# Performance work log

Measured on AMD Instinct MI355X. Metric: run time of the kernel, lower is better.

The kernel has to match this reference:

```python
import jax, jax.numpy as jnp
import numpy as np

B, N, D, H = 4, 16384, 64, 8
MIN_FREQ = 1.0 / 64.0
SCALE = 1.0
EPS = 1e-5


def layernorm(x):
    # LayerNorm over last (head-feature) dim, no affine, biased variance (torch default)
    m = jnp.mean(x, axis=-1, keepdims=True)
    v = jnp.mean(jnp.square(x - m), axis=-1, keepdims=True)
    return (x - m) * jax.lax.rsqrt(v + EPS)


def rope_freqs(pos):
    # pos: [b, n, 1] 1-D coordinates -> freqs [b, n, D]
    inv_freq = 1.0 / (10000.0 ** (jnp.arange(0, D, 2, dtype=jnp.float32) / D))  # [D/2]
    t = pos[..., 0] * (SCALE / MIN_FREQ)                                         # [b, n]
    f = t[..., None] * inv_freq                                                  # [b, n, D/2]
    return jnp.concatenate([f, f], axis=-1)                                      # [b, n, D]


def rotate_half(x):
    x1, x2 = jnp.split(x, 2, axis=-1)
    return jnp.concatenate([-x2, x1], axis=-1)


def apply_rope(x, freqs):
    # x: [b, h, n, d], freqs: [b, n, d]
    c = jnp.cos(freqs)[:, None]
    s = jnp.sin(freqs)[:, None]
    return x * c + rotate_half(x) * s


def setup_inputs() -> dict:
    key = jax.random.key(0)
    ks = jax.random.split(key, 6)
    gain = 1.0 / D
    return {
        "x": jax.random.normal(ks[0], (B, N, D), dtype=jnp.float32),
        "pos": jax.random.uniform(ks[1], (B, N, 1), dtype=jnp.float32),
        "Wq": jax.random.normal(ks[2], (D, D * H), dtype=jnp.float32) * gain,
        "Wk": jax.random.normal(ks[3], (D, D * H), dtype=jnp.float32) * gain,
        "Wv": jax.random.normal(ks[4], (D, D * H), dtype=jnp.float32) * gain,
        "Wo": jax.random.normal(ks[5], (D * H, D), dtype=jnp.float32) * gain,
    }


def reference(x, pos, Wq, Wk, Wv, Wo):
    b, n, _ = x.shape

    def proj(W):
        # [b, n, d] @ [d, h*d] -> [b, h, n, d]
        y = jnp.einsum("bnd,de->bne", x, W)
        return y.reshape(b, n, H, D).transpose(0, 2, 1, 3)

    q, k, v = proj(Wq), proj(Wk), proj(Wv)

    # galerkin: layernorm k and v (no mask path)
    k = layernorm(k)
    v = layernorm(v)

    # RoPE on q, k
    freqs = rope_freqs(pos)
    q = apply_rope(q, freqs)
    k = apply_rope(k, freqs)

    # linear attention: z = q @ (k^T v) / n
    kv = jnp.einsum("bhnd,bhne->bhde", k, v)          # [b, h, d, d]
    z = jnp.einsum("bhnd,bhde->bhne", q, kv) / n      # [b, h, n, d]
    z = z.transpose(0, 2, 1, 3).reshape(b, n, H * D)  # [b, n, h*d]

    return jnp.einsum("bne,ed->bnd", z, Wo)           # out_proj (dropout=0)
```

## Files before the change

### kernel.cpp

```cpp
#include <hip/hip_runtime.h>

#define B_ 4
#define N_ 16384
#define D_ 64
#define H_ 8
#define E_ 512
#define NCHUNK 32
#define NTILES (N_ / 64)

typedef __attribute__((ext_vector_type(8))) short short8;
typedef __attribute__((ext_vector_type(4))) float f32x4;
typedef __attribute__((ext_vector_type(2))) unsigned int uint32x2;

__device__ __forceinline__ unsigned short f2b(float f) {
    unsigned u = __float_as_uint(f);
    return (unsigned short)((u + 0x7fffu + ((u >> 16) & 1u)) >> 16);
}

__device__ __forceinline__ unsigned cvtpk(float a, float b) {
    unsigned r;
    asm("v_cvt_pk_bf16_f32 %0, %1, %2" : "=v"(r) : "v"(a), "v"(b));
    return r;
}

template<int CTRL>
__device__ __forceinline__ float dppadd(float x) {
    int y = __builtin_amdgcn_update_dpp(0, __float_as_int(x), CTRL, 0xF, 0xF, true);
    return x + __int_as_float(y);
}
__device__ __forceinline__ float rowsum16(float x) {
    x = dppadd<0xB1>(x);
    x = dppadd<0x4E>(x);
    x = dppadd<0x141>(x);
    x = dppadd<0x140>(x);
    return x;
}

__global__ __launch_bounds__(256) void k_prep(
    const float* __restrict__ x,
    const float* __restrict__ Wq, const float* __restrict__ Wk,
    const float* __restrict__ Wv,
    unsigned short* __restrict__ WqB, unsigned short* __restrict__ WkB,
    unsigned short* __restrict__ WvB,
    unsigned short* __restrict__ xblob)
{
    const int bid = blockIdx.x, tid = threadIdx.x;
    if (bid < 384) {
        int mat = bid >> 7, sub = bid & 127;
        const float* src = (mat == 0) ? Wq : (mat == 1) ? Wk : Wv;
        unsigned short* dst = (mat == 0) ? WqB : (mat == 1) ? WkB : WvB;
        int id = sub * 256 + tid;
        int kin = id >> 9, f = id & 511;
        int h = f >> 6, feat = f & 63;
        int nt = feat >> 4, cc = feat & 15;
        int half = kin >> 5, qd = (kin >> 3) & 3, e = kin & 7;
        dst[(size_t)h * 4096 + (((nt * 2 + half) * 64 + qd * 16 + cc) * 8) + e]
            = f2b(src[id]);
        return;
    }
    int idx = (bid - 384) * 256 + tid;
    int lane = idx & 63, fr = (idx >> 6) & 1, tb = (idx >> 7) & 1023, b = idx >> 17;
    int cc = lane & 15, qd = lane >> 4;
    const float* src = &x[((size_t)b * N_ + tb * 16 + cc) * 64 + fr * 32 + qd * 8];
    float4 v0 = *(const float4*)src;
    float4 v1 = *(const float4*)(src + 4);
    ushort4 u0, u1;
    u0.x = f2b(v0.x); u0.y = f2b(v0.y); u0.z = f2b(v0.z); u0.w = f2b(v0.w);
    u1.x = f2b(v1.x); u1.y = f2b(v1.y); u1.z = f2b(v1.z); u1.w = f2b(v1.w);
    *(ushort4*)&xblob[(size_t)idx * 8]     = u0;
    *(ushort4*)&xblob[(size_t)idx * 8 + 4] = u1;
}

__global__ __launch_bounds__(256, 4) void k_kv(
    const unsigned short* __restrict__ xblob,
    const float* __restrict__ pos,
    const unsigned short* __restrict__ WkB,
    const unsigned short* __restrict__ WvB,
    float* __restrict__ kv_part)
{
    const int b = blockIdx.z, h = blockIdx.y, chunk = blockIdx.x;
    const int tid  = threadIdx.x;
    const int lane = tid & 63;
    const int w    = tid >> 6;
    const int c    = lane & 15;
    const int quad = lane >> 4;
    const int m0   = w * 16;

    __shared__ unsigned short kbuf[64 * 72];
    __shared__ unsigned short vbuf[64 * 72];
    __shared__ unsigned short wkl[4096];
    __shared__ unsigned short wvl[4096];

    {
        const float4* srcK = (const float4*)(WkB + (size_t)h * 4096);
        const float4* srcV = (const float4*)(WvB + (size_t)h * 4096);
        float4* dstK = (float4*)wkl;
        float4* dstV = (float4*)wvl;
        #pragma unroll
        for (int i = 0; i < 2; ++i) {
            dstK[tid + i * 256] = srcK[tid + i * 256];
            dstV[tid + i * 256] = srcV[tid + i * 256];
        }
    }

    const float invf_lo = exp2f(-0.4152410118609203f * (float)c);
    const float invf_hi = invf_lo * 0.01f;

    f32x4 akv[4];
    #pragma unroll
    for (int nt = 0; nt < 4; ++nt) akv[nt] = (f32x4){0.f, 0.f, 0.f, 0.f};

    short8 a0, a1;
    float tp[4];
    {
        int tb = chunk * 4 + w;
        const unsigned short* xb = xblob + (size_t)((b * 1024 + tb) * 2) * 512 + lane * 8;
        a0 = *(const short8*)&xb[0];
        a1 = *(const short8*)&xb[512];
        #pragma unroll
        for (int r = 0; r < 4; ++r)
            tp[r] = pos[(size_t)b * N_ + chunk * 64 + m0 + quad * 4 + r] * 64.0f;
    }
    __syncthreads();

    for (int tile = chunk; tile < NTILES; tile += NCHUNK) {
        f32x4 ak[4], av[4];
        #pragma unroll
        for (int nt = 0; nt < 4; ++nt) {
            short8 bk0 = *(const short8*)&wkl[(nt * 2 + 0) * 512 + lane * 8];
            short8 bk1 = *(const short8*)&wkl[(nt * 2 + 1) * 512 + lane * 8];
            f32x4 z = {0.f, 0.f, 0.f, 0.f};
            z = __builtin_amdgcn_mfma_f32_16x16x32_bf16(a0, bk0, z, 0, 0, 0);
            ak[nt] = __builtin_amdgcn_mfma_f32_16x16x32_bf16(a1, bk1, z, 0, 0, 0);
            short8 bv0 = *(const short8*)&wvl[(nt * 2 + 0) * 512 + lane * 8];
            short8 bv1 = *(const short8*)&wvl[(nt * 2 + 1) * 512 + lane * 8];
            f32x4 y = {0.f, 0.f, 0.f, 0.f};
            y = __builtin_amdgcn_mfma_f32_16x16x32_bf16(a0, bv0, y, 0, 0, 0);
            av[nt] = __builtin_amdgcn_mfma_f32_16x16x32_bf16(a1, bv1, y, 0, 0, 0);
        }

        float cl[4], sl[4], ch[4], sh[4];
        #pragma unroll
        for (int r = 0; r < 4; ++r) {
            float al = tp[r] * invf_lo, ah = tp[r] * invf_hi;
            cl[r] = __cosf(al); sl[r] = __sinf(al);
            ch[r] = __cosf(ah); sh[r] = __sinf(ah);
        }

        const int tn = tile + NCHUNK;
        if (tn < NTILES) {
            int tb = tn * 4 + w;
            const unsigned short* xb = xblob + (size_t)((b * 1024 + tb) * 2) * 512 + lane * 8;
            a0 = *(const short8*)&xb[0];
            a1 = *(const short8*)&xb[512];
            #pragma unroll
            for (int r = 0; r < 4; ++r)
                tp[r] = pos[(size_t)b * N_ + tn * 64 + m0 + quad * 4 + r] * 64.0f;
        }
        __builtin_amdgcn_sched_barrier(0);

        #pragma unroll
        for (int r = 0; r < 4; ++r) {
            float sk  = ak[0][r] + ak[1][r] + ak[2][r] + ak[3][r];
            float sk2 = ak[0][r]*ak[0][r] + ak[1][r]*ak[1][r] + ak[2][r]*ak[2][r] + ak[3][r]*ak[3][r];
            float sv  = av[0][r] + av[1][r] + av[2][r] + av[3][r];
            float sv2 = av[0][r]*av[0][r] + av[1][r]*av[1][r] + av[2][r]*av[2][r] + av[3][r]*av[3][r];
            sk = rowsum16(sk); sk2 = rowsum16(sk2);
            sv = rowsum16(sv); sv2 = rowsum16(sv2);
            float mk = sk * (1.0f / 64.0f);
            float rk = rsqrtf(sk2 * (1.0f / 64.0f) - mk * mk + 1e-5f);
            float mv = sv * (1.0f / 64.0f);
            float rv = rsqrtf(sv2 * (1.0f / 64.0f) - mv * mv + 1e-5f);
            #pragma unroll
            for (int nt = 0; nt < 4; ++nt) {
                ak[nt][r] = (ak[nt][r] - mk) * rk;
                av[nt][r] = (av[nt][r] - mv) * rv;
            }
        }

        #pragma unroll
        for (int r = 0; r < 4; ++r) {
            float lo0 = ak[0][r], hi0 = ak[2][r];
            ak[0][r] = lo0 * cl[r] - hi0 * sl[r];
            ak[2][r] = hi0 * cl[r] + lo0 * sl[r];
            float lo1 = ak[1][r], hi1 = ak[3][r];
            ak[1][r] = lo1 * ch[r] - hi1 * sh[r];
            ak[3][r] = hi1 * ch[r] + lo1 * sh[r];
        }

        __syncthreads();

        #pragma unroll
        for (int nt = 0; nt < 4; ++nt) {
            uint32x2 kk, vv;
            kk[0] = cvtpk(ak[nt][0], ak[nt][1]);
            kk[1] = cvtpk(ak[nt][2], ak[nt][3]);
            vv[0] = cvtpk(av[nt][0], av[nt][1]);
            vv[1] = cvtpk(av[nt][2], av[nt][3]);
            *(uint32x2*)&kbuf[(nt * 16 + c) * 72 + m0 + quad * 4] = kk;
            *(uint32x2*)&vbuf[(nt * 16 + c) * 72 + m0 + quad * 4] = vv;
        }
        __syncthreads();

        short8 ka0 = *(const short8*)&kbuf[(m0 + c) * 72 + quad * 8];
        short8 ka1 = *(const short8*)&kbuf[(m0 + c) * 72 + 32 + quad * 8];
        #pragma unroll
        for (int nt = 0; nt < 4; ++nt) {
            short8 vb0 = *(const short8*)&vbuf[(nt * 16 + c) * 72 + quad * 8];
            short8 vb1 = *(const short8*)&vbuf[(nt * 16 + c) * 72 + 32 + quad * 8];
            akv[nt] = __builtin_amdgcn_mfma_f32_16x16x32_bf16(ka0, vb0, akv[nt], 0, 0, 0);
            akv[nt] = __builtin_amdgcn_mfma_f32_16x16x32_bf16(ka1, vb1, akv[nt], 0, 0, 0);
        }
    }

    float* dst = kv_part + ((size_t)(b * H_ + h) * NCHUNK + chunk) * 4096;
    #pragma unroll
    for (int nt = 0; nt < 4; ++nt)
        #pragma unroll
        for (int r = 0; r < 4; ++r)
            dst[(size_t)(16 * w + quad * 4 + r) * 64 + nt * 16 + c] = akv[nt][r];
}

__global__ __launch_bounds__(256) void k_m(
    const float* __restrict__ kv_part,
    const float* __restrict__ Wo,
    unsigned short* __restrict__ MTB)
{
    const int h = blockIdx.x, b = blockIdx.y, s = blockIdx.z;
    const int tid = threadIdx.x;
    __shared__ float kvs[8 * 65];
    __shared__ float wos[64 * 68];

    const float* src = kv_part + (size_t)(b * H_ + h) * NCHUNK * 4096 + s * 512;
    #pragma unroll
    for (int k = 0; k < 2; ++k) {
        int idx = tid + k * 256;
        float ssum = 0.f;
        #pragma unroll 8
        for (int ch = 0; ch < NCHUNK; ++ch) ssum += src[(size_t)ch * 4096 + idx];
        kvs[(idx >> 6) * 65 + (idx & 63)] = ssum;
    }
    for (int i = tid; i < 1024; i += 256) {
        int dp = i >> 4, j4 = (i & 15) * 4;
        *(float4*)&wos[dp * 68 + j4] = *(const float4*)&Wo[(size_t)(h * 64 + dp) * 64 + j4];
    }
    __syncthreads();

    const float inv_n = 1.0f / (float)N_;
    unsigned short* dst = MTB + (size_t)(b * H_ + h) * 4096;
    const int half = s >> 2, qd = s & 3;
    #pragma unroll
    for (int k = 0; k < 2; ++k) {
        int idx = tid + k * 256;
        int dl = idx >> 6, j = idx & 63;
        float acc = 0.f;
        #pragma unroll 8
        for (int e = 0; e < 64; ++e)
            acc += kvs[dl * 65 + e] * wos[e * 68 + j];
        int nt = j >> 4, cc = j & 15;
        dst[(((nt * 2 + half) * 64 + qd * 16 + cc) * 8) + dl] = f2b(acc * inv_n);
    }
}

__global__ __launch_bounds__(256, 3) void k_out(
    const unsigned short* __restrict__ xblob,
    const float* __restrict__ pos,
    const unsigned short* __restrict__ WqB,
    const unsigned short* __restrict__ MTB,
    float* __restrict__ out)
{
    const int b = blockIdx.y;
    const int n0 = blockIdx.x * 64;
    const int tid  = threadIdx.x;
    const int lane = tid & 63;
    const int w    = tid >> 6;
    const int c    = lane & 15;
    const int quad = lane >> 4;
    const int m0   = w * 16;

    __shared__ unsigned short qbuf[64 * 72];

    const int tb = blockIdx.x * 4 + w;
    const unsigned short* xb = xblob + (size_t)((b * 1024 + tb) * 2) * 512 + lane * 8;
    short8 a0 = *(const short8*)&xb[0];
    short8 a1 = *(const short8*)&xb[512];

    const unsigned short* wq0 = WqB + (size_t)lane * 8;
    const unsigned short* mt0 = MTB + (size_t)(b * H_) * 4096 + (size_t)lane * 8;
    short8 W[8], Mt[8];
    #pragma unroll
    for (int fr = 0; fr < 8; ++fr) W[fr]  = *(const short8*)&wq0[fr * 512];
    #pragma unroll
    for (int fr = 0; fr < 8; ++fr) Mt[fr] = *(const short8*)&mt0[fr * 512];
    __builtin_amdgcn_sched_barrier(0);

    const float invf_lo = exp2f(-0.4152410118609203f * (float)c);
    const float invf_hi = invf_lo * 0.01f;
    float csl[4], snl[4], csh[4], snh[4];
    #pragma unroll
    for (int r = 0; r < 4; ++r) {
        float tpv = pos[(size_t)b * N_ + n0 + m0 + quad * 4 + r] * 64.0f;
        float al = tpv * invf_lo, ah = tpv * invf_hi;
        csl[r] = __cosf(al); snl[r] = __sinf(al);
        csh[r] = __cosf(ah); snh[r] = __sinf(ah);
    }

    f32x4 oacc[4];
    #pragma unroll
    for (int nt = 0; nt < 4; ++nt) oacc[nt] = (f32x4){0.f, 0.f, 0.f, 0.f};

    #pragma unroll
    for (int h = 0; h < H_; ++h) {
        f32x4 aq[4];
        #pragma unroll
        for (int nt = 0; nt < 4; ++nt) {
            f32x4 z = {0.f, 0.f, 0.f, 0.f};
            z = __builtin_amdgcn_mfma_f32_16x16x32_bf16(a0, W[nt * 2 + 0], z, 0, 0, 0);
            aq[nt] = __builtin_amdgcn_mfma_f32_16x16x32_bf16(a1, W[nt * 2 + 1], z, 0, 0, 0);
        }

        if (h < H_ - 1) {
            #pragma unroll
            for (int fr = 0; fr < 8; ++fr)
                W[fr] = *(const short8*)&wq0[(size_t)(h + 1) * 4096 + fr * 512];
        }
        __builtin_amdgcn_sched_barrier(0);

        #pragma unroll
        for (int r = 0; r < 4; ++r) {
            float lo0 = aq[0][r], hi0 = aq[2][r];
            aq[0][r] = lo0 * csl[r] - hi0 * snl[r];
            aq[2][r] = hi0 * csl[r] + lo0 * snl[r];
            float lo1 = aq[1][r], hi1 = aq[3][r];
            aq[1][r] = lo1 * csh[r] - hi1 * snh[r];
            aq[3][r] = hi1 * csh[r] + lo1 * snh[r];
        }

        #pragma unroll
        for (int nt = 0; nt < 4; ++nt) {
            unsigned q01 = cvtpk(aq[nt][0], aq[nt][1]);
            unsigned q23 = cvtpk(aq[nt][2], aq[nt][3]);
            int base = (m0 + quad * 4) * 72 + nt * 16 + c;
            qbuf[base]       = (unsigned short)q01;
            qbuf[base + 72]  = (unsigned short)(q01 >> 16);
            qbuf[base + 144] = (unsigned short)q23;
            qbuf[base + 216] = (unsigned short)(q23 >> 16);
        }

        short8 qa0 = *(const short8*)&qbuf[(m0 + c) * 72 + quad * 8];
        short8 qa1 = *(const short8*)&qbuf[(m0 + c) * 72 + 32 + quad * 8];
        #pragma unroll
        for (int nt = 0; nt < 4; ++nt) {
            oacc[nt] = __builtin_amdgcn_mfma_f32_16x16x32_bf16(qa0, Mt[nt * 2 + 0], oacc[nt], 0, 0, 0);
            oacc[nt] = __builtin_amdgcn_mfma_f32_16x16x32_bf16(qa1, Mt[nt * 2 + 1], oacc[nt], 0, 0, 0);
        }

        if (h < H_ - 1) {
            #pragma unroll
            for (int fr = 0; fr < 8; ++fr)
                Mt[fr] = *(const short8*)&mt0[(size_t)(h + 1) * 4096 + fr * 512];
        }
        __builtin_amdgcn_sched_barrier(0);
    }

    #pragma unroll
    for (int nt = 0; nt < 4; ++nt)
        #pragma unroll
        for (int r = 0; r < 4; ++r)
            out[(size_t)(b * N_ + n0 + m0 + quad * 4 + r) * 64 + nt * 16 + c] = oacc[nt][r];
}

extern "C" void kernel_launch(void* const* d_in, const int* in_sizes, int n_in,
                              void* d_out, int out_size, void* d_ws, size_t ws_size,
                              hipStream_t stream)
{
    const float* x   = (const float*)d_in[0];
    const float* pos = (const float*)d_in[1];
    const float* Wq  = (const float*)d_in[2];
    const float* Wk  = (const float*)d_in[3];
    const float* Wv  = (const float*)d_in[4];
    const float* Wo  = (const float*)d_in[5];
    float* out = (float*)d_out;

    char* ws = (char*)d_ws;
    float* kv_part        = (float*)ws;
    unsigned short* MTB   = (unsigned short*)(ws + 16777216);
    unsigned short* WqB   = (unsigned short*)(ws + 17039360);
    unsigned short* WkB   = (unsigned short*)(ws + 17104896);
    unsigned short* WvB   = (unsigned short*)(ws + 17170432);
    unsigned short* xblob = (unsigned short*)(ws + 17235968);

    k_prep<<<dim3(2432), 256, 0, stream>>>(x, Wq, Wk, Wv,
                                           WqB, WkB, WvB, xblob);
    k_kv  <<<dim3(NCHUNK, H_, B_), 256, 0, stream>>>(xblob, pos, WkB, WvB, kv_part);
    k_m   <<<dim3(H_, B_, 8), 256, 0, stream>>>(kv_part, Wo, MTB);
    k_out <<<dim3(NTILES, B_), 256, 0, stream>>>(xblob, pos, WqB, MTB, out);
}
```

Measured before the change: 142.0 us.

## Run two tile streams per 512-thread kv block and reduce partials in LDS

The k_kv kernel now launches 512-thread blocks holding two independent groups of four waves. Each group processes its own strided tile stream with separate LDS k/v buffers, which raises the number of tile streams from 32 to 48 per (b,h). The two groups' kv accumulators are summed through LDS before writing, so there are only 24 partials per head, which shrinks the k_m reduction and the workspace. The grid gets fewer, larger blocks, and the two groups share __syncthreads barriers, which may couple their progress.

After: 190.0 us. +33.8%, slower.

```diff
diff --git a/kernel.cpp b/kernel.cpp
--- a/kernel.cpp
+++ b/kernel.cpp
@@ -5,7 +5,8 @@
 #define D_ 64
 #define H_ 8
 #define E_ 512
-#define NCHUNK 32
+#define NPART 24
+#define TSTREAMS 48
 #define NTILES (N_ / 64)
 
 typedef __attribute__((ext_vector_type(8))) short short8;
@@ -71,37 +72,30 @@
     *(ushort4*)&xblob[(size_t)idx * 8 + 4] = u1;
 }
 
-__global__ __launch_bounds__(256, 4) void k_kv(
+__global__ __launch_bounds__(512, 6) void k_kv(
     const unsigned short* __restrict__ xblob,
     const float* __restrict__ pos,
     const unsigned short* __restrict__ WkB,
     const unsigned short* __restrict__ WvB,
     float* __restrict__ kv_part)
 {
-    const int b = blockIdx.z, h = blockIdx.y, chunk = blockIdx.x;
+    const int b = blockIdx.z, h = blockIdx.y, bx = blockIdx.x;
     const int tid  = threadIdx.x;
     const int lane = tid & 63;
     const int w    = tid >> 6;
+    const int g    = w >> 2;
+    const int wl   = w & 3;
     const int c    = lane & 15;
     const int quad = lane >> 4;
-    const int m0   = w * 16;
-
-    __shared__ unsigned short kbuf[64 * 72];
-    __shared__ unsigned short vbuf[64 * 72];
+    const int m0   = wl * 16;
+
+    __shared__ unsigned short kbuf[2][64 * 72];
+    __shared__ unsigned short vbuf[2][64 * 72];
     __shared__ unsigned short wkl[4096];
     __shared__ unsigned short wvl[4096];
 
-    {
-        const float4* srcK = (const float4*)(WkB + (size_t)h * 4096);
-        const float4* srcV = (const float4*)(WvB + (size_t)h * 4096);
-        float4* dstK = (float4*)wkl;
-        float4* dstV = (float4*)wvl;
-        #pragma unroll
-        for (int i = 0; i < 2; ++i) {
-            dstK[tid + i * 256] = srcK[tid + i * 256];
-            dstV[tid + i * 256] = srcV[tid + i * 256];
-        }
-    }
+    ((float4*)wkl)[tid] = ((const float4*)(WkB + (size_t)h * 4096))[tid];
+    ((float4*)wvl)[tid] = ((const float4*)(WvB + (size_t)h * 4096))[tid];
 
     const float invf_lo = exp2f(-0.4152410118609203f * (float)c);
     const float invf_hi = invf_lo * 0.01f;
@@ -110,20 +104,21 @@
     #pragma unroll
     for (int nt = 0; nt < 4; ++nt) akv[nt] = (f32x4){0.f, 0.f, 0.f, 0.f};
 
+    const int tile0 = bx * 2 + g;
     short8 a0, a1;
     float tp[4];
     {
-        int tb = chunk * 4 + w;
+        int tb = tile0 * 4 + wl;
         const unsigned short* xb = xblob + (size_t)((b * 1024 + tb) * 2) * 512 + lane * 8;
         a0 = *(const short8*)&xb[0];
         a1 = *(const short8*)&xb[512];
         #pragma unroll
         for (int r = 0; r < 4; ++r)
-            tp[r] = pos[(size_t)b * N_ + chunk * 64 + m0 + quad * 4 + r] * 64.0f;
+            tp[r] = pos[(size_t)b * N_ + tile0 * 64 + m0 + quad * 4 + r] * 64.0f;
     }
     __syncthreads();
 
-    for (int tile = chunk; tile < NTILES; tile += NCHUNK) {
+    for (int tile = tile0; tile < NTILES; tile += TSTREAMS) {
         f32x4 ak[4], av[4];
         #pragma unroll
         for (int nt = 0; nt < 4; ++nt) {
@@ -147,9 +142,9 @@
             ch[r] = __cosf(ah); sh[r] = __sinf(ah);
         }
 
-        const int tn = tile + NCHUNK;
+        const int tn = tile + TSTREAMS;
         if (tn < NTILES) {
-            int tb = tn * 4 + w;
+            int tb = tn * 4 + wl;
             const unsigned short* xb = xblob + (size_t)((b * 1024 + tb) * 2) * 512 + lane * 8;
             a0 = *(const short8*)&xb[0];
             a1 = *(const short8*)&xb[512];
@@ -197,28 +192,42 @@
             kk[1] = cvtpk(ak[nt][2], ak[nt][3]);
             vv[0] = cvtpk(av[nt][0], av[nt][1]);
             vv[1] = cvtpk(av[nt][2], av[nt][3]);
-            *(uint32x2*)&kbuf[(nt * 16 + c) * 72 + m0 + quad * 4] = kk;
-            *(uint32x2*)&vbuf[(nt * 16 + c) * 72 + m0 + quad * 4] = vv;
+            *(uint32x2*)&kbuf[g][(nt * 16 + c) * 72 + m0 + quad * 4] = kk;
+            *(uint32x2*)&vbuf[g][(nt * 16 + c) * 72 + m0 + quad * 4] = vv;
         }
         __syncthreads();
 
-        short8 ka0 = *(const short8*)&kbuf[(m0 + c) * 72 + quad * 8];
-        short8 ka1 = *(const short8*)&kbuf[(m0 + c) * 72 + 32 + quad * 8];
-        #pragma unroll
-        for (int nt = 0; nt < 4; ++nt) {
-            short8 vb0 = *(const short8*)&vbuf[(nt * 16 + c) * 72 + quad * 8];
-            short8 vb1 = *(const short8*)&vbuf[(nt * 16 + c) * 72 + 32 + quad * 8];
+        short8 ka0 = *(const short8*)&kbuf[g][(m0 + c) * 72 + quad * 8];
+        short8 ka1 = *(const short8*)&kbuf[g][(m0 + c) * 72 + 32 + quad * 8];
+        #pragma unroll
+        for (int nt = 0; nt < 4; ++nt) {
+            short8 vb0 = *(const short8*)&vbuf[g][(nt * 16 + c) * 72 + quad * 8];
+            short8 vb1 = *(const short8*)&vbuf[g][(nt * 16 + c) * 72 + 32 + quad * 8];
             akv[nt] = __builtin_amdgcn_mfma_f32_16x16x32_bf16(ka0, vb0, akv[nt], 0, 0, 0);
             akv[nt] = __builtin_amdgcn_mfma_f32_16x16x32_bf16(ka1, vb1, akv[nt], 0, 0, 0);
         }
     }
 
-    float* dst = kv_part + ((size_t)(b * H_ + h) * NCHUNK + chunk) * 4096;
-    #pragma unroll
-    for (int nt = 0; nt < 4; ++nt)
-        #pragma unroll
-        for (int r = 0; r < 4; ++r)
-            dst[(size_t)(16 * w + quad * 4 + r) * 64 + nt * 16 + c] = akv[nt][r];
+    __syncthreads();
+    float* fbuf = (float*)kbuf;
+    if (g == 1) {
+        #pragma unroll
+        for (int nt = 0; nt < 4; ++nt)
+            #pragma unroll
+            for (int r = 0; r < 4; ++r)
+                fbuf[(size_t)(16 * wl + quad * 4 + r) * 64 + nt * 16 + c] = akv[nt][r];
+    }
+    __syncthreads();
+    if (g == 0) {
+        float* dst = kv_part + ((size_t)(b * H_ + h) * NPART + bx) * 4096;
+        #pragma unroll
+        for (int nt = 0; nt < 4; ++nt)
+            #pragma unroll
+            for (int r = 0; r < 4; ++r) {
+                int idx = (16 * wl + quad * 4 + r) * 64 + nt * 16 + c;
+                dst[idx] = akv[nt][r] + fbuf[idx];
+            }
+    }
 }
 
 __global__ __launch_bounds__(256) void k_m(
@@ -231,13 +240,13 @@
     __shared__ float kvs[8 * 65];
     __shared__ float wos[64 * 68];
 
-    const float* src = kv_part + (size_t)(b * H_ + h) * NCHUNK * 4096 + s * 512;
+    const float* src = kv_part + (size_t)(b * H_ + h) * NPART * 4096 + s * 512;
     #pragma unroll
     for (int k = 0; k < 2; ++k) {
         int idx = tid + k * 256;
         float ssum = 0.f;
-        #pragma unroll 8
-        for (int ch = 0; ch < NCHUNK; ++ch) ssum += src[(size_t)ch * 4096 + idx];
+        #pragma unroll 6
+        for (int ch = 0; ch < NPART; ++ch) ssum += src[(size_t)ch * 4096 + idx];
         kvs[(idx >> 6) * 65 + (idx & 63)] = ssum;
     }
     for (int i = tid; i < 1024; i += 256) {
@@ -384,15 +393,15 @@
 
     char* ws = (char*)d_ws;
     float* kv_part        = (float*)ws;
-    unsigned short* MTB   = (unsigned short*)(ws + 16777216);
-    unsigned short* WqB   = (unsigned short*)(ws + 17039360);
-    unsigned short* WkB   = (unsigned short*)(ws + 17104896);
-    unsigned short* WvB   = (unsigned short*)(ws + 17170432);
-    unsigned short* xblob = (unsigned short*)(ws + 17235968);
+    unsigned short* MTB   = (unsigned short*)(ws + 12582912);
+    unsigned short* WqB   = (unsigned short*)(ws + 12845056);
+    unsigned short* WkB   = (unsigned short*)(ws + 12910592);
+    unsigned short* WvB   = (unsigned short*)(ws + 12976128);
+    unsigned short* xblob = (unsigned short*)(ws + 13041664);
 
     k_prep<<<dim3(2432), 256, 0, stream>>>(x, Wq, Wk, Wv,
                                            WqB, WkB, WvB, xblob);
-    k_kv  <<<dim3(NCHUNK, H_, B_), 256, 0, stream>>>(xblob, pos, WkB, WvB, kv_part);
+    k_kv  <<<dim3(NPART, H_, B_), 512, 0, stream>>>(xblob, pos, WkB, WvB, kv_part);
     k_m   <<<dim3(H_, B_, 8), 256, 0, stream>>>(kv_part, Wo, MTB);
     k_out <<<dim3(NTILES, B_), 256, 0, stream>>>(xblob, pos, WqB, MTB, out);
 }
```
